# Optimization experiments

Hardware: AMD Instinct MI355X
Metric: run time of the kernel (lower is better)

The kernel has to match this reference:

```python
import jax, jax.numpy as jnp
import numpy as np

B, P, T, R, A = 16384, 3, 2, 3, 3   # batch, n_players, teammates, rivals, action_dim
HID = [1024, 512]
ENC_OUT = 64
RIVAL_START = 9 * 9 + 12 * P       # 117, as in the torch module
NEG_SLOPE = 0.01                    # nn.LeakyReLU default


def _linpack(key, k, din, dout):
    # PyTorch nn.Linear default init: U(-1/sqrt(din), 1/sqrt(din))
    kw, kb = jax.random.split(key)
    bound = 1.0 / np.sqrt(din)
    W = jax.random.uniform(kw, (k, din, dout), jnp.float32, -bound, bound)
    b = jax.random.uniform(kb, (k, dout), jnp.float32, -bound, bound)
    return W, b


def setup_inputs() -> dict:
    key = jax.random.key(0)
    ks = jax.random.split(key, 16)
    obs = jax.random.normal(ks[0], (B, P, 144), jnp.float32)
    act = jax.random.normal(ks[1], (B, P, A), jnp.float32)
    # stacked per-segment encoder weights (grouped small GEMMs)
    Wp1, bp1 = _linpack(ks[2], 9, 2 + A, 32)
    Wp2, bp2 = _linpack(ks[3], 9, 32, ENC_OUT)
    Wt1, bt1 = _linpack(ks[4], T, 12, 32)
    Wt2, bt2 = _linpack(ks[5], T, 32, ENC_OUT)
    Wr1, br1 = _linpack(ks[6], R, 9, 32)
    Wr2, br2 = _linpack(ks[7], R, 32, ENC_OUT)
    # q head: [P*896] -> 1024 -> 512 -> P
    din = P * (9 + T + R) * ENC_OUT
    Wq1, bq1 = _linpack(ks[8], 1, din, HID[0]);  Wq1, bq1 = Wq1[0], bq1[0]
    Wq2, bq2 = _linpack(ks[9], 1, HID[0], HID[1]); Wq2, bq2 = Wq2[0], bq2[0]
    Wq3, bq3 = _linpack(ks[10], 1, HID[1], P);   Wq3, bq3 = Wq3[0], bq3[0]
    return dict(obs=obs, act=act,
                Wp1=Wp1, bp1=bp1, Wp2=Wp2, bp2=bp2,
                Wt1=Wt1, bt1=bt1, Wt2=Wt2, bt2=bt2,
                Wr1=Wr1, br1=br1, Wr2=Wr2, br2=br2,
                Wq1=Wq1, bq1=bq1, Wq2=Wq2, bq2=bq2, Wq3=Wq3, bq3=bq3)


def _enc2(x, W1, b1, W2, b2):
    # x: [B, P, K, din]; W1: [K, din, 32]; W2: [K, 32, 64] -> [B, P, K, 64]
    lrelu = lambda v: jax.nn.leaky_relu(v, NEG_SLOPE)
    h = lrelu(jnp.einsum('bpki,kio->bpko', x, W1) + b1)
    return lrelu(jnp.einsum('bpkh,kho->bpko', h, W2) + b2)


def reference(obs, act, Wp1, bp1, Wp2, bp2, Wt1, bt1, Wt2, bt2,
              Wr1, br1, Wr2, br2, Wq1, bq1, Wq2, bq2, Wq3, bq3):
    b = obs.shape[0]
    # prop segments: obs[:, :, 2i:2i+2] concat act  -> [B, P, 9, 2+A]
    x_prop = jnp.concatenate(
        [obs[:, :, :18].reshape(b, P, 9, 2),
         jnp.broadcast_to(act[:, :, None, :], (b, P, 9, A))], axis=-1)
    x_team = obs[:, :, 18:18 + 12 * T].reshape(b, P, T, 12)
    x_riv = obs[:, :, RIVAL_START:RIVAL_START + 9 * R].reshape(b, P, R, 9)
    ep = _enc2(x_prop, Wp1, bp1, Wp2, bp2)   # [B, P, 9, 64]
    et = _enc2(x_team, Wt1, bt1, Wt2, bt2)   # [B, P, T, 64]
    er = _enc2(x_riv, Wr1, br1, Wr2, br2)    # [B, P, R, 64]
    enc = jnp.concatenate([ep, et, er], axis=2).reshape(b, -1)  # [B, P*14*64]
    # q head: ReLU hidden activations, identity output
    h = jax.nn.relu(enc @ Wq1 + bq1)
    h = jax.nn.relu(h @ Wq2 + bq2)
    return h @ Wq3 + bq3                      # [B, P]
```

## Files before the change

### kernel.cpp

```cpp
#include <hip/hip_runtime.h>
#include <hip/hip_bf16.h>
#include <cstdint>

typedef __bf16 bf16x8 __attribute__((ext_vector_type(8)));
typedef float f32x4 __attribute__((ext_vector_type(4)));

__device__ __forceinline__ void gld16(const __bf16* g, __bf16* lds) {
    __builtin_amdgcn_global_load_lds(
        (__attribute__((address_space(1))) void*)(uintptr_t)g,
        (__attribute__((address_space(3))) void*)(uint32_t)(uintptr_t)lds,
        16, 0, 0);
}

__global__ __launch_bounds__(256) void transpose_bf16_k(const float* __restrict__ in,
                                                        __bf16* __restrict__ out,
                                                        int R, int C) {
    __shared__ float t[64][65];
    const int r0 = blockIdx.x * 64, c0 = blockIdx.y * 64;
    const int tid = threadIdx.x;
#pragma unroll
    for (int i = 0; i < 16; i++) {
        int idx = i * 256 + tid;
        int rr = idx >> 6, cc = idx & 63;
        t[rr][cc] = in[(size_t)(r0 + rr) * C + (c0 + cc)];
    }
    __syncthreads();
#pragma unroll
    for (int i = 0; i < 16; i++) {
        int idx = i * 256 + tid;
        int rr = idx >> 6, cc = idx & 63;
        out[(size_t)(c0 + rr) * R + (r0 + cc)] = (__bf16)t[cc][rr];
    }
}

__global__ __launch_bounds__(256) void pack_weights(const float* __restrict__ Wp1, const float* __restrict__ bp1,
                                                    const float* __restrict__ Wp2, const float* __restrict__ bp2,
                                                    const float* __restrict__ Wt1, const float* __restrict__ bt1,
                                                    const float* __restrict__ Wt2, const float* __restrict__ bt2,
                                                    const float* __restrict__ Wr1, const float* __restrict__ br1,
                                                    const float* __restrict__ Wr2, const float* __restrict__ br2,
                                                    float* __restrict__ w1p, __bf16* __restrict__ w2t) {
    const int s = blockIdx.x, tid = threadIdx.x;
    int ks, din, w1off;
    const float *W1, *B1, *W2, *B2;
    if (s < 9)      { ks = s;      din = 5;  w1off = s * 160;
                      W1 = Wp1; B1 = bp1; W2 = Wp2; B2 = bp2; }
    else if (s < 11){ ks = s - 9;  din = 12; w1off = 1440 + ks * 384;
                      W1 = Wt1; B1 = bt1; W2 = Wt2; B2 = bt2; }
    else            { ks = s - 11; din = 9;  w1off = 2208 + ks * 288;
                      W1 = Wr1; B1 = br1; W2 = Wr2; B2 = br2; }
    W1 += ks * din * 32; B1 += ks * 32; W2 += ks * 2048; B2 += ks * 64;
    for (int i = tid; i < din * 32; i += 256) w1p[w1off + i] = W1[i];
    if (tid < 32) w1p[3072 + s * 32 + tid] = B1[tid];
    if (tid < 64) w1p[3520 + s * 64 + tid] = B2[tid];
    for (int i = tid; i < 2048; i += 256) {
        const int o = i >> 5, k = i & 31;
        w2t[s * 2048 + i] = (__bf16)W2[k * 64 + o];
    }
}

__global__ __launch_bounds__(192) void enc_fused(const float* __restrict__ obs,
                                                 const float* __restrict__ act,
                                                 const float* __restrict__ w1p,
                                                 const __bf16* __restrict__ w2t,
                                                 __bf16* __restrict__ enc) {
    __shared__ float sW[4416];
    __shared__ __bf16 sH[2][192 * 40];
    const int tid = threadIdx.x;
    for (int i = tid; i < 4416; i += 192) sW[i] = w1p[i];
    const int row = blockIdx.x * 192 + tid;
    const float* orow = obs + (size_t)row * 144;
    const float a0 = act[row * 3], a1 = act[row * 3 + 1], a2 = act[row * 3 + 2];
    const int wv = tid >> 6, lane = tid & 63;
    const int fr = lane & 15, kq = lane >> 4;
    const int rq = (lane >> 4) << 2;
    __syncthreads();
    int buf = 0;

    auto l2 = [&](int s) {
        __syncthreads();
        bf16x8 bfr[4], afr[4];
#pragma unroll
        for (int n = 0; n < 4; n++)
            bfr[n] = *(const bf16x8*)&w2t[(s * 64 + n * 16 + fr) * 32 + kq * 8];
#pragma unroll
        for (int m = 0; m < 4; m++)
            afr[m] = *(const bf16x8*)&sH[buf][(wv * 64 + m * 16 + fr) * 40 + kq * 8];
        f32x4 acc[4][4] = {};
#pragma unroll
        for (int m = 0; m < 4; m++)
#pragma unroll
            for (int n = 0; n < 4; n++)
                acc[m][n] = __builtin_amdgcn_mfma_f32_16x16x32_bf16(afr[m], bfr[n], acc[m][n], 0, 0, 0);
        const float* b2 = sW + 3520 + s * 64;
#pragma unroll
        for (int m = 0; m < 4; m++) {
            const size_t rG = (size_t)blockIdx.x * 192 + wv * 64 + m * 16 + rq;
#pragma unroll
            for (int n = 0; n < 4; n++) {
                const float bv = b2[n * 16 + fr];
#pragma unroll
                for (int rg = 0; rg < 4; rg++) {
                    float v = acc[m][n][rg] + bv;
                    v = fmaxf(v, 0.01f * v);
                    enc[(rG + rg) * 896 + s * 64 + n * 16 + fr] = (__bf16)v;
                }
            }
        }
        buf ^= 1;
    };

#define L1(DIN, W1OFF, SGI, XLOAD)                                   \
    {                                                                \
        float x[DIN];                                                \
        XLOAD;                                                       \
        const float* w1 = sW + (W1OFF);                              \
        const float* b1 = sW + 3072 + (SGI) * 32;                    \
        float h[32];                                                 \
        _Pragma("unroll") for (int o = 0; o < 32; o++) {             \
            float a_ = b1[o];                                        \
            _Pragma("unroll") for (int i = 0; i < DIN; i++)          \
                a_ += x[i] * w1[i * 32 + o];                         \
            h[o] = fmaxf(a_, 0.01f * a_);                            \
        }                                                            \
        __bf16* hr = &sH[buf][tid * 40];                             \
        _Pragma("unroll") for (int sl = 0; sl < 4; sl++) {           \
            bf16x8 t_;                                               \
            _Pragma("unroll") for (int j = 0; j < 8; j++)            \
                t_[j] = (__bf16)h[sl * 8 + j];                       \
            *(bf16x8*)&hr[sl * 8] = t_;                              \
        }                                                            \
    }

    for (int k = 0; k < 9; k++) {
        L1(5, k * 160, k,
           { x[0] = orow[2 * k]; x[1] = orow[2 * k + 1]; x[2] = a0; x[3] = a1; x[4] = a2; })
        l2(k);
    }
    for (int k = 0; k < 2; k++) {
        L1(12, 1440 + k * 384, 9 + k,
           { _Pragma("unroll") for (int i = 0; i < 12; i++) x[i] = orow[18 + 12 * k + i]; })
        l2(9 + k);
    }
    for (int k = 0; k < 3; k++) {
        L1(9, 2208 + k * 288, 11 + k,
           { _Pragma("unroll") for (int i = 0; i < 9; i++) x[i] = orow[117 + 9 * k + i]; })
        l2(11 + k);
    }
#undef L1
}

template <int NB>
__global__ __launch_bounds__(512, 2) void gemm256_relu(const __bf16* __restrict__ Ag,
                                                       const __bf16* __restrict__ Btg,
                                                       const float* __restrict__ bias,
                                                       __bf16* __restrict__ Cg,
                                                       int N, int K, int lgn) {
    __shared__ __align__(16) __bf16 ldsA[2][2][128 * 64];
    __shared__ __align__(16) __bf16 ldsB[2][2][NB * 64 * 64];
    const int tid = threadIdx.x;
    const int wid = tid >> 6, lane = tid & 63;
    const int wm = wid >> 2, wn = wid & 3;
    const int fr = lane & 15, kq = lane >> 4;

    const int chunk = gridDim.x >> 3;
    const int wg = (blockIdx.x & 7) * chunk + (blockIdx.x >> 3);
    const int bn = wg & ((1 << lgn) - 1), bm = wg >> lgn;

    const int c0 = tid, c1 = tid + 512;
    const int r0 = c0 >> 3, s0 = (c0 & 7) ^ (r0 & 7);
    const int r1 = c1 >> 3, s1 = (c1 & 7) ^ (r1 & 7);
    const size_t aH = (size_t)128 * K;
    const size_t bH = (size_t)(NB * 64) * K;
    const __bf16* aB0 = Ag + (size_t)(bm * 256 + r0) * K + s0 * 8;
    const __bf16* aB1 = Ag + (size_t)(bm * 256 + r1) * K + s1 * 8;
    const __bf16* bB0 = Btg + (size_t)(bn * (NB * 128) + r0) * K + s0 * 8;
    const __bf16* bB1 = Btg + (size_t)(bn * (NB * 128) + r1) * K + s1 * 8;

    f32x4 acc[2][2][4][NB] = {};
    bf16x8 a0[4][2], a1[4][2], b0[NB][2], b1[NB][2];

#define STAGE_A(BUF, H, KO)                                   \
    do {                                                      \
        __bf16* d_ = &ldsA[BUF][H][0];                        \
        gld16(aB0 + (H)*aH + (KO), d_ + c0 * 8);              \
        gld16(aB1 + (H)*aH + (KO), d_ + c1 * 8);              \
    } while (0)
#define STAGE_B(BUF, H, KO)                                   \
    do {                                                      \
        __bf16* d_ = &ldsB[BUF][H][0];                        \
        gld16(bB0 + (H)*bH + (KO), d_ + c0 * 8);              \
        if constexpr (NB == 2) gld16(bB1 + (H)*bH + (KO), d_ + c1 * 8); \
    } while (0)

#define LDFA(BUF, H, ROW, KS) \
    (*(const bf16x8*)&ldsA[BUF][H][(ROW) * 64 + ((((KS)*4 + kq) ^ ((ROW)&7)) * 8)])
#define LDFB(BUF, H, ROW, KS) \
    (*(const bf16x8*)&ldsB[BUF][H][(ROW) * 64 + ((((KS)*4 + kq) ^ ((ROW)&7)) * 8)])

#define LOAD_A(BUF, H, DST)                                   \
    _Pragma("unroll") for (int m = 0; m < 4; m++)             \
        _Pragma("unroll") for (int ks = 0; ks < 2; ks++)      \
            DST[m][ks] = LDFA(BUF, H, wm * 64 + m * 16 + fr, ks);
#define LOAD_B(BUF, H, DST)                                   \
    _Pragma("unroll") for (int n = 0; n < NB; n++)            \
        _Pragma("unroll") for (int ks = 0; ks < 2; ks++)      \
            DST[n][ks] = LDFB(BUF, H, wn * (NB * 16) + n * 16 + fr, ks);

#define MM(Q, R, AR, BR)                                      \
    __builtin_amdgcn_s_setprio(1);                            \
    _Pragma("unroll") for (int ks = 0; ks < 2; ks++)          \
        _Pragma("unroll") for (int m = 0; m < 4; m++)         \
            _Pragma("unroll") for (int n = 0; n < NB; n++)    \
                acc[Q][R][m][n] = __builtin_amdgcn_mfma_f32_16x16x32_bf16( \
                    AR[m][ks], BR[n][ks], acc[Q][R][m][n], 0, 0, 0); \
    __builtin_amdgcn_s_setprio(0);

#define SB0 __builtin_amdgcn_sched_barrier(0)
#define BAR __builtin_amdgcn_s_barrier()
#define LGKM_B1                                               \
    if constexpr (NB == 2) asm volatile("s_waitcnt lgkmcnt(4)" ::: "memory"); \
    else asm volatile("s_waitcnt lgkmcnt(2)" ::: "memory");
#define LGKM(NSTR) asm volatile("s_waitcnt lgkmcnt(" NSTR ")" ::: "memory")
#define VMW(NSTR) asm volatile("s_waitcnt vmcnt(" NSTR ")" ::: "memory")
#define VMW2(N2, N1)                                          \
    if constexpr (NB == 2) VMW(#N2); else VMW(#N1);

    const int NT = K >> 6;

    STAGE_A(0, 0, 0);
    STAGE_B(0, 0, 0);
    STAGE_B(0, 1, 0);
    STAGE_A(0, 1, 0);
    VMW("2");
    BAR;
    LOAD_A(0, 0, a0)
    LOAD_B(0, 0, b0)
    SB0;

    for (int t = 0; t < NT - 1; ++t) {
        const int buf = t & 1, nb = buf ^ 1;
        const int kO = (t + 1) << 6;

        STAGE_A(nb, 0, kO);
        STAGE_B(nb, 0, kO);
        VMW2(4, 3);
        LOAD_B(buf, 1, b1)
        SB0;
        BAR;
        LGKM_B1;
        SB0;
        MM(0, 0, a0, b0)

        STAGE_B(nb, 1, kO);
        STAGE_A(nb, 1, kO);
        LOAD_A(buf, 1, a1)
        SB0;
        BAR;
        LGKM("8");
        SB0;
        MM(0, 1, a0, b1)

        BAR;
        LGKM("0");
        SB0;
        MM(1, 0, a1, b0)

        VMW("2");
        BAR;
        LOAD_A(nb, 0, a0)
        LOAD_B(nb, 0, b0)
        SB0;
        MM(1, 1, a1, b1)
    }

    {
        const int buf = (NT - 1) & 1;
        VMW("0");
        LOAD_B(buf, 1, b1)
        SB0;
        BAR;
        LGKM_B1;
        SB0;
        MM(0, 0, a0, b0)

        LOAD_A(buf, 1, a1)
        SB0;
        BAR;
        LGKM("8");
        SB0;
        MM(0, 1, a0, b1)

        BAR;
        LGKM("0");
        SB0;
        MM(1, 0, a1, b0)

        MM(1, 1, a1, b1)
    }

    const int cc = lane & 15, rr = (lane >> 4) << 2;
#pragma unroll
    for (int q = 0; q < 2; q++)
#pragma unroll
        for (int r2 = 0; r2 < 2; r2++)
#pragma unroll
            for (int m = 0; m < 4; m++)
#pragma unroll
                for (int n = 0; n < NB; n++) {
                    const int colG = bn * (NB * 128) + r2 * (NB * 64) + wn * (NB * 16) + n * 16 + cc;
                    const int rowG = bm * 256 + q * 128 + wm * 64 + m * 16 + rr;
                    const float bv = bias[colG];
#pragma unroll
                    for (int reg = 0; reg < 4; reg++) {
                        float v = acc[q][r2][m][n][reg] + bv;
                        v = fmaxf(v, 0.0f);
                        Cg[(size_t)(rowG + reg) * N + colG] = (__bf16)v;
                    }
                }
#undef STAGE_A
#undef STAGE_B
#undef LDFA
#undef LDFB
#undef LOAD_A
#undef LOAD_B
#undef MM
#undef SB0
#undef BAR
#undef LGKM_B1
#undef LGKM
#undef VMW
#undef VMW2
}

__global__ __launch_bounds__(256) void head_kernel(const __bf16* __restrict__ h2,
                                                   const float* __restrict__ Wq3,
                                                   const float* __restrict__ bq3,
                                                   float* __restrict__ out) {
    const int wave = threadIdx.x >> 6, lane = threadIdx.x & 63;
    const int row = blockIdx.x * 4 + wave;
    const bf16x8 hv = *(const bf16x8*)(h2 + (size_t)row * 512 + lane * 8);
    float s0 = 0.f, s1 = 0.f, s2 = 0.f;
#pragma unroll
    for (int i = 0; i < 8; i++) {
        const float hf = (float)hv[i];
        const int k = lane * 8 + i;
        s0 += hf * Wq3[k * 3 + 0];
        s1 += hf * Wq3[k * 3 + 1];
        s2 += hf * Wq3[k * 3 + 2];
    }
#pragma unroll
    for (int off = 32; off > 0; off >>= 1) {
        s0 += __shfl_xor(s0, off);
        s1 += __shfl_xor(s1, off);
        s2 += __shfl_xor(s2, off);
    }
    if (lane == 0) {
        float* o = out + (size_t)row * 3;
        o[0] = s0 + bq3[0];
        o[1] = s1 + bq3[1];
        o[2] = s2 + bq3[2];
    }
}

extern "C" void kernel_launch(void* const* d_in, const int* in_sizes, int n_in,
                              void* d_out, int out_size, void* d_ws, size_t ws_size,
                              hipStream_t stream) {
    const float* obs = (const float*)d_in[0];
    const float* act = (const float*)d_in[1];
    const float* Wp1 = (const float*)d_in[2];  const float* bp1 = (const float*)d_in[3];
    const float* Wp2 = (const float*)d_in[4];  const float* bp2 = (const float*)d_in[5];
    const float* Wt1 = (const float*)d_in[6];  const float* bt1 = (const float*)d_in[7];
    const float* Wt2 = (const float*)d_in[8];  const float* bt2 = (const float*)d_in[9];
    const float* Wr1 = (const float*)d_in[10]; const float* br1 = (const float*)d_in[11];
    const float* Wr2 = (const float*)d_in[12]; const float* br2 = (const float*)d_in[13];
    const float* Wq1 = (const float*)d_in[14]; const float* bq1 = (const float*)d_in[15];
    const float* Wq2 = (const float*)d_in[16]; const float* bq2 = (const float*)d_in[17];
    const float* Wq3 = (const float*)d_in[18]; const float* bq3 = (const float*)d_in[19];
    float* out = (float*)d_out;

    char* ws = (char*)d_ws;
    __bf16* enc = (__bf16*)(ws);
    __bf16* h1  = (__bf16*)(ws + 88080384);
    __bf16* h2  = (__bf16*)(ws + 88080384 + 33554432);
    __bf16* w1t = (__bf16*)(ws + 138412032);
    __bf16* w2t = (__bf16*)(ws + 143917056);
    float*  w1p = (float*)(ws + 144965632);
    __bf16* w2e = (__bf16*)(ws + 144983296);

    pack_weights<<<14, 256, 0, stream>>>(Wp1, bp1, Wp2, bp2, Wt1, bt1, Wt2, bt2,
                                         Wr1, br1, Wr2, br2, w1p, w2e);
    transpose_bf16_k<<<dim3(2688 / 64, 1024 / 64), 256, 0, stream>>>(Wq1, w1t, 2688, 1024);
    transpose_bf16_k<<<dim3(1024 / 64, 512 / 64), 256, 0, stream>>>(Wq2, w2t, 1024, 512);

    enc_fused<<<256, 192, 0, stream>>>(obs, act, w1p, w2e, enc);

    gemm256_relu<2><<<dim3(256), 512, 0, stream>>>(enc, w1t, bq1, h1, 1024, 2688, 2);
    gemm256_relu<1><<<dim3(256), 512, 0, stream>>>(h1, w2t, bq2, h2, 512, 1024, 2);
    head_kernel<<<16384 / 4, 256, 0, stream>>>(h2, Wq3, bq3, out);
}
```

Baseline: 162.0 us.

## Split encoder layer-1 work across 4 threads per row and reschedule GEMM barriers

The encoder kernel now assigns four threads to each batch row instead of one. Each thread computes 8 of the 32 hidden outputs, and each wave runs a single 16-row MFMA tile instead of four. Blocks shrink to 64 rows and the grid grows from 256 to 768, which should raise occupancy and cut per-thread register use and serial work. Separately, the main GEMM loop is reordered with extra barriers and earlier LDS fragment loads to overlap differently, at the cost of more synchronisation.

After: 153.8 us. 1.05x faster.

```diff
diff --git a/kernel.cpp b/kernel.cpp
--- a/kernel.cpp
+++ b/kernel.cpp
@@ -59,52 +59,45 @@
     }
 }
 
-__global__ __launch_bounds__(192) void enc_fused(const float* __restrict__ obs,
+__global__ __launch_bounds__(256) void enc_fused(const float* __restrict__ obs,
                                                  const float* __restrict__ act,
                                                  const float* __restrict__ w1p,
                                                  const __bf16* __restrict__ w2t,
                                                  __bf16* __restrict__ enc) {
     __shared__ float sW[4416];
-    __shared__ __bf16 sH[2][192 * 40];
+    __shared__ __bf16 sH[2][64 * 40];
     const int tid = threadIdx.x;
-    for (int i = tid; i < 4416; i += 192) sW[i] = w1p[i];
-    const int row = blockIdx.x * 192 + tid;
+    for (int i = tid; i < 4416; i += 256) sW[i] = w1p[i];
+    const int rloc = tid >> 2, q = tid & 3;
+    const int row = blockIdx.x * 64 + rloc;
     const float* orow = obs + (size_t)row * 144;
     const float a0 = act[row * 3], a1 = act[row * 3 + 1], a2 = act[row * 3 + 2];
     const int wv = tid >> 6, lane = tid & 63;
     const int fr = lane & 15, kq = lane >> 4;
-    const int rq = (lane >> 4) << 2;
     __syncthreads();
     int buf = 0;
 
     auto l2 = [&](int s) {
         __syncthreads();
-        bf16x8 bfr[4], afr[4];
+        bf16x8 bfr[4];
 #pragma unroll
         for (int n = 0; n < 4; n++)
             bfr[n] = *(const bf16x8*)&w2t[(s * 64 + n * 16 + fr) * 32 + kq * 8];
-#pragma unroll
-        for (int m = 0; m < 4; m++)
-            afr[m] = *(const bf16x8*)&sH[buf][(wv * 64 + m * 16 + fr) * 40 + kq * 8];
-        f32x4 acc[4][4] = {};
-#pragma unroll
-        for (int m = 0; m < 4; m++)
-#pragma unroll
-            for (int n = 0; n < 4; n++)
-                acc[m][n] = __builtin_amdgcn_mfma_f32_16x16x32_bf16(afr[m], bfr[n], acc[m][n], 0, 0, 0);
+        const bf16x8 afr = *(const bf16x8*)&sH[buf][(wv * 16 + fr) * 40 + kq * 8];
+        f32x4 acc[4] = {};
+#pragma unroll
+        for (int n = 0; n < 4; n++)
+            acc[n] = __builtin_amdgcn_mfma_f32_16x16x32_bf16(afr, bfr[n], acc[n], 0, 0, 0);
         const float* b2 = sW + 3520 + s * 64;
-#pragma unroll
-        for (int m = 0; m < 4; m++) {
-            const size_t rG = (size_t)blockIdx.x * 192 + wv * 64 + m * 16 + rq;
-#pragma unroll
-            for (int n = 0; n < 4; n++) {
-                const float bv = b2[n * 16 + fr];
-#pragma unroll
-                for (int rg = 0; rg < 4; rg++) {
-                    float v = acc[m][n][rg] + bv;
-                    v = fmaxf(v, 0.01f * v);
-                    enc[(rG + rg) * 896 + s * 64 + n * 16 + fr] = (__bf16)v;
-                }
+        const size_t rG = (size_t)blockIdx.x * 64 + wv * 16 + kq * 4;
+#pragma unroll
+        for (int n = 0; n < 4; n++) {
+            const float bv = b2[n * 16 + fr];
+#pragma unroll
+            for (int rg = 0; rg < 4; rg++) {
+                float v = acc[n][rg] + bv;
+                v = fmaxf(v, 0.01f * v);
+                enc[(rG + rg) * 896 + s * 64 + n * 16 + fr] = (__bf16)v;
             }
         }
         buf ^= 1;
@@ -116,20 +109,15 @@
         XLOAD;                                                       \
         const float* w1 = sW + (W1OFF);                              \
         const float* b1 = sW + 3072 + (SGI) * 32;                    \
-        float h[32];                                                 \
-        _Pragma("unroll") for (int o = 0; o < 32; o++) {             \
+        bf16x8 t_;                                                   \
+        _Pragma("unroll") for (int j = 0; j < 8; j++) {              \
+            const int o = q * 8 + j;                                 \
             float a_ = b1[o];                                        \
             _Pragma("unroll") for (int i = 0; i < DIN; i++)          \
                 a_ += x[i] * w1[i * 32 + o];                         \
-            h[o] = fmaxf(a_, 0.01f * a_);                            \
+            t_[j] = (__bf16)fmaxf(a_, 0.01f * a_);                   \
         }                                                            \
-        __bf16* hr = &sH[buf][tid * 40];                             \
-        _Pragma("unroll") for (int sl = 0; sl < 4; sl++) {           \
-            bf16x8 t_;                                               \
-            _Pragma("unroll") for (int j = 0; j < 8; j++)            \
-                t_[j] = (__bf16)h[sl * 8 + j];                       \
-            *(bf16x8*)&hr[sl * 8] = t_;                              \
-        }                                                            \
+        *(bf16x8*)&sH[buf][rloc * 40 + q * 8] = t_;                  \
     }
 
     for (int k = 0; k < 9; k++) {
@@ -218,10 +206,9 @@
 
 #define SB0 __builtin_amdgcn_sched_barrier(0)
 #define BAR __builtin_amdgcn_s_barrier()
-#define LGKM_B1                                               \
-    if constexpr (NB == 2) asm volatile("s_waitcnt lgkmcnt(4)" ::: "memory"); \
-    else asm volatile("s_waitcnt lgkmcnt(2)" ::: "memory");
 #define LGKM(NSTR) asm volatile("s_waitcnt lgkmcnt(" NSTR ")" ::: "memory")
+#define LGKM2(N2, N1)                                         \
+    if constexpr (NB == 2) LGKM(#N2); else LGKM(#N1);
 #define VMW(NSTR) asm volatile("s_waitcnt vmcnt(" NSTR ")" ::: "memory")
 #define VMW2(N2, N1)                                          \
     if constexpr (NB == 2) VMW(#N2); else VMW(#N1);
@@ -248,9 +235,10 @@
         LOAD_B(buf, 1, b1)
         SB0;
         BAR;
-        LGKM_B1;
+        LGKM2(4, 2);
         SB0;
         MM(0, 0, a0, b0)
+        BAR;
 
         STAGE_B(nb, 1, kO);
         STAGE_A(nb, 1, kO);
@@ -260,18 +248,22 @@
         LGKM("8");
         SB0;
         MM(0, 1, a0, b1)
-
-        BAR;
-        LGKM("0");
+        BAR;
+
+        VMW("2");
+        SB0;
+        BAR;
+        LOAD_A(nb, 0, a0)
+        SB0;
+        LGKM("8");
         SB0;
         MM(1, 0, a1, b0)
-
-        VMW("2");
-        BAR;
-        LOAD_A(nb, 0, a0)
+        BAR;
+
         LOAD_B(nb, 0, b0)
         SB0;
         MM(1, 1, a1, b1)
+        BAR;
     }
 
     {
@@ -280,9 +272,10 @@
         LOAD_B(buf, 1, b1)
         SB0;
         BAR;
-        LGKM_B1;
+        LGKM2(4, 2);
         SB0;
         MM(0, 0, a0, b0)
+        BAR;
 
         LOAD_A(buf, 1, a1)
         SB0;
@@ -290,12 +283,11 @@
         LGKM("8");
         SB0;
         MM(0, 1, a0, b1)
-
-        BAR;
+        BAR;
+
         LGKM("0");
         SB0;
         MM(1, 0, a1, b0)
-
         MM(1, 1, a1, b1)
     }
 
@@ -327,8 +319,8 @@
 #undef MM
 #undef SB0
 #undef BAR
-#undef LGKM_B1
 #undef LGKM
+#undef LGKM2
 #undef VMW
 #undef VMW2
 }
@@ -393,7 +385,7 @@
     transpose_bf16_k<<<dim3(2688 / 64, 1024 / 64), 256, 0, stream>>>(Wq1, w1t, 2688, 1024);
     transpose_bf16_k<<<dim3(1024 / 64, 512 / 64), 256, 0, stream>>>(Wq2, w2t, 1024, 512);
 
-    enc_fused<<<256, 192, 0, stream>>>(obs, act, w1p, w2e, enc);
+    enc_fused<<<768, 256, 0, stream>>>(obs, act, w1p, w2e, enc);
 
     gemm256_relu<2><<<dim3(256), 512, 0, stream>>>(enc, w1t, bq1, h1, 1024, 2688, 2);
     gemm256_relu<1><<<dim3(256), 512, 0, stream>>>(h1, w2t, bq2, h2, 512, 1024, 2);
```
